# Kernel tuning notes

Hardware: AMD Instinct MI355X
Metric: run time of the kernel (lower is better)

## Reference

```python
import jax, jax.numpy as jnp
import numpy as np


def _ln(x, g, b, eps=1e-5):
    m = jnp.mean(x, axis=-1, keepdims=True)
    v = jnp.mean((x - m) ** 2, axis=-1, keepdims=True)
    return (x - m) / jnp.sqrt(v + eps) * g + b


def _win_part(x, ws):
    # (B,H,W,C) -> (B*nW, ws*ws, C)
    B, H, W, C = x.shape
    x = x.reshape(B, H // ws, ws, W // ws, ws, C)
    x = jnp.transpose(x, (0, 1, 3, 2, 4, 5))
    return x.reshape(-1, ws * ws, C)


def _win_rev(w, ws, H, W):
    # (B*nW, ws, ws, C) -> (B,H,W,C)
    C = w.shape[-1]
    B = w.shape[0] // ((H // ws) * (W // ws))
    x = w.reshape(B, H // ws, W // ws, ws, ws, C)
    x = jnp.transpose(x, (0, 1, 3, 2, 4, 5))
    return x.reshape(B, H, W, C)


def _build_mask(H, W, ws, ss):
    # standard Swin SW-MSA mask, built with numpy at trace time (static shapes)
    img = np.zeros((H, W), np.float32)
    cnt = 0
    for hs in (slice(0, -ws), slice(-ws, -ss), slice(-ss, None)):
        for wsl in (slice(0, -ws), slice(-ws, -ss), slice(-ss, None)):
            img[hs, wsl] = cnt
            cnt += 1
    mw = img.reshape(H // ws, ws, W // ws, ws).transpose(0, 2, 1, 3).reshape(-1, ws * ws)
    diff = mw[:, None, :] - mw[:, :, None]  # (nW, N, N)
    return jnp.asarray(np.where(diff != 0, -np.inf, 0.0).astype(np.float32))


def _swin_block(x, H, W, ws, shift, heads, p):
    B, L, C = x.shape
    hd = C // heads
    N = ws * ws
    shortcut = x
    xg = _ln(x, p['ln1_g'], p['ln1_b']).reshape(B, H, W, C)
    mask = None
    if shift > 0:
        xg = jnp.roll(xg, shift=(-shift, -shift), axis=(1, 2))
        mask = _build_mask(H, W, ws, shift)
    xw = _win_part(xg, ws)  # (B_, N, C)
    qkv = xw @ p['qkv_w'] + p['qkv_b']  # (B_, N, 3C)
    qkv = jnp.transpose(qkv.reshape(-1, N, 3, heads, hd), (2, 0, 3, 1, 4))
    q, k, v = qkv[0] * (hd ** -0.5), qkv[1], qkv[2]  # (B_, h, N, hd)
    attn = jnp.einsum('bhnd,bhmd->bhnm', q, k)
    if mask is not None:
        nW = mask.shape[0]
        attn = attn.reshape(B, nW, heads, N, N) + mask[None, :, None]
        attn = attn.reshape(-1, heads, N, N)
    attn = jax.nn.softmax(attn, axis=-1)
    out = jnp.einsum('bhnm,bhmd->bhnd', attn, v)
    out = jnp.transpose(out, (0, 2, 1, 3)).reshape(-1, N, C)
    out = out @ p['proj_w'] + p['proj_b']
    xg = _win_rev(out.reshape(-1, ws, ws, C), ws, H, W)
    if shift > 0:
        xg = jnp.roll(xg, shift=(shift, shift), axis=(1, 2))
    x = shortcut + xg.reshape(B, L, C)
    h = jax.nn.gelu(_ln(x, p['ln2_g'], p['ln2_b']) @ p['fc1_w'] + p['fc1_b'], approximate=False)
    return x + (h @ p['fc2_w'] + p['fc2_b'])


def _patch_merge(x, H, W, g, b, w):
    B, L, C = x.shape
    xg = x.reshape(B, H, W, C)
    xc = jnp.concatenate([xg[:, 0::2, 0::2], xg[:, 1::2, 0::2], xg[:, 0::2, 1::2], xg[:, 1::2, 1::2]], axis=-1)
    xc = xc.reshape(B, (H // 2) * (W // 2), 4 * C)
    return _ln(xc, g, b) @ w


def setup_inputs() -> dict:
    key = jax.random.key(0)
    ks = jax.random.split(key, 16)
    B, H, W, C = 8, 96, 96, 128
    s = 0.02
    d = {'x': jax.random.normal(ks[0], (B, H * W, C), jnp.float32)}
    i = 1
    for pre in ('a_', 'b_'):
        d[pre + 'ln1_g'] = jnp.ones((C,), jnp.float32)
        d[pre + 'ln1_b'] = jnp.zeros((C,), jnp.float32)
        d[pre + 'qkv_w'] = s * jax.random.normal(ks[i], (C, 3 * C), jnp.float32); i += 1
        d[pre + 'qkv_b'] = jnp.zeros((3 * C,), jnp.float32)
        d[pre + 'proj_w'] = s * jax.random.normal(ks[i], (C, C), jnp.float32); i += 1
        d[pre + 'proj_b'] = jnp.zeros((C,), jnp.float32)
        d[pre + 'ln2_g'] = jnp.ones((C,), jnp.float32)
        d[pre + 'ln2_b'] = jnp.zeros((C,), jnp.float32)
        d[pre + 'fc1_w'] = s * jax.random.normal(ks[i], (C, 4 * C), jnp.float32); i += 1
        d[pre + 'fc1_b'] = jnp.zeros((4 * C,), jnp.float32)
        d[pre + 'fc2_w'] = s * jax.random.normal(ks[i], (4 * C, C), jnp.float32); i += 1
        d[pre + 'fc2_b'] = jnp.zeros((C,), jnp.float32)
    d['mln_g'] = jnp.ones((4 * C,), jnp.float32)
    d['mln_b'] = jnp.zeros((4 * C,), jnp.float32)
    d['red_w'] = s * jax.random.normal(ks[i], (4 * C, 2 * C), jnp.float32)
    d['H'] = H
    d['W'] = W
    return d


def reference(x, a_ln1_g, a_ln1_b, a_qkv_w, a_qkv_b, a_proj_w, a_proj_b, a_ln2_g, a_ln2_b, a_fc1_w, a_fc1_b, a_fc2_w, a_fc2_b, b_ln1_g, b_ln1_b, b_qkv_w, b_qkv_b, b_proj_w, b_proj_b, b_ln2_g, b_ln2_b, b_fc1_w, b_fc1_b, b_fc2_w, b_fc2_b, mln_g, mln_b, red_w, H, W):
    heads, ws = 4, 8
    pa = dict(ln1_g=a_ln1_g, ln1_b=a_ln1_b, qkv_w=a_qkv_w, qkv_b=a_qkv_b, proj_w=a_proj_w, proj_b=a_proj_b, ln2_g=a_ln2_g, ln2_b=a_ln2_b, fc1_w=a_fc1_w, fc1_b=a_fc1_b, fc2_w=a_fc2_w, fc2_b=a_fc2_b)
    pb = dict(ln1_g=b_ln1_g, ln1_b=b_ln1_b, qkv_w=b_qkv_w, qkv_b=b_qkv_b, proj_w=b_proj_w, proj_b=b_proj_b, ln2_g=b_ln2_g, ln2_b=b_ln2_b, fc1_w=b_fc1_w, fc1_b=b_fc1_b, fc2_w=b_fc2_w, fc2_b=b_fc2_b)
    x = _swin_block(x, H, W, ws, 0, heads, pa)          # W-MSA
    x = _swin_block(x, H, W, ws, ws // 2, heads, pb)     # SW-MSA
    return _patch_merge(x, H, W, mln_g, mln_b, red_w)    # (B, HW/4, 2C)
```

## Files before the change

### kernel.cpp

```cpp
#include <hip/hip_runtime.h>
#include <hip/hip_bf16.h>

typedef __bf16 bf16_t;
typedef __bf16 bf16x2 __attribute__((ext_vector_type(2)));
typedef __bf16 bf16x8 __attribute__((ext_vector_type(8)));
typedef float floatx4 __attribute__((ext_vector_type(4)));

#define NTOK 73728
#define LNS 136

__device__ __forceinline__ void gl16(const bf16_t* g, bf16_t* l) {
    __builtin_amdgcn_global_load_lds((const __attribute__((address_space(1))) void*)g,
                                     (__attribute__((address_space(3))) void*)l, 16, 0, 0);
}

__device__ __forceinline__ void stage_ln(const float* __restrict__ src, const float* __restrict__ g,
                                         const float* __restrict__ bta, bf16_t* lnA, int tid) {
    int r = tid >> 2, q = tid & 3;
    const float* rowp = src + (size_t)r * 128 + q * 32;
    float4 v[8];
    float s = 0.0f, sq = 0.0f;
    #pragma unroll
    for (int i = 0; i < 8; i++) {
        v[i] = *(const float4*)(rowp + i * 4);
        s += v[i].x + v[i].y + v[i].z + v[i].w;
        sq += v[i].x * v[i].x + v[i].y * v[i].y + v[i].z * v[i].z + v[i].w * v[i].w;
    }
    s += __shfl_xor(s, 1, 64); sq += __shfl_xor(sq, 1, 64);
    s += __shfl_xor(s, 2, 64); sq += __shfl_xor(sq, 2, 64);
    float m = s * (1.0f / 128.0f);
    float inv = rsqrtf(sq * (1.0f / 128.0f) - m * m + 1e-5f);
    bf16_t* dst = lnA + r * LNS + q * 32;
    #pragma unroll
    for (int i = 0; i < 4; i++) {
        float4 a = v[2 * i], b = v[2 * i + 1];
        float4 g0 = *(const float4*)(g + q * 32 + i * 8);
        float4 g1 = *(const float4*)(g + q * 32 + i * 8 + 4);
        float4 b0 = *(const float4*)(bta + q * 32 + i * 8);
        float4 b1 = *(const float4*)(bta + q * 32 + i * 8 + 4);
        bf16x8 o;
        o[0] = (bf16_t)((a.x - m) * inv * g0.x + b0.x);
        o[1] = (bf16_t)((a.y - m) * inv * g0.y + b0.y);
        o[2] = (bf16_t)((a.z - m) * inv * g0.z + b0.z);
        o[3] = (bf16_t)((a.w - m) * inv * g0.w + b0.w);
        o[4] = (bf16_t)((b.x - m) * inv * g1.x + b1.x);
        o[5] = (bf16_t)((b.y - m) * inv * g1.y + b1.y);
        o[6] = (bf16_t)((b.z - m) * inv * g1.z + b1.z);
        o[7] = (bf16_t)((b.w - m) * inv * g1.w + b1.w);
        *(bf16x8*)(dst + i * 8) = o;
    }
}

struct TPack {
    const float* src[9];
    bf16_t* dst[9];
    int K[9], N[9];
};
__global__ __launch_bounds__(256) void kconv_frag(TPack p) {
    int seg = blockIdx.y;
    int K = p.K[seg], N = p.N[seg];
    int idx = blockIdx.x * 256 + threadIdx.x;
    if (idx >= K * N) return;
    int j = idx & 7;
    int lane = (idx >> 3) & 63;
    int blk = idx >> 9;
    int tilesK = K >> 5;
    int ntile = blk / tilesK, kc = blk - ntile * tilesK;
    int n = ntile * 16 + (lane & 15);
    int k = kc * 32 + (lane >> 4) * 8 + j;
    p.dst[seg][idx] = (bf16_t)p.src[seg][(size_t)k * N + n];
}

__global__ __launch_bounds__(256, 4) void kqkv(const float* __restrict__ X,
                                               const float* __restrict__ g, const float* __restrict__ bta,
                                               const bf16_t* __restrict__ Wf,
                                               const float* __restrict__ bias,
                                               bf16_t* __restrict__ out) {
    alignas(16) __shared__ bf16_t lA[64 * LNS];
    const int tid = threadIdx.x;
    const int rowA = blockIdx.y * 64;
    const int rowB = blockIdx.x * 128;
    stage_ln(X + (size_t)rowA * 128, g, bta, lA, tid);
    __syncthreads();
    const int lane = tid & 63, wv = tid >> 6;
    const int wm = (wv & 1) * 32, wn = (wv >> 1) * 64;
    const int frow = lane & 15, fq = lane >> 4;
    const bf16_t* pw = Wf + (size_t)((rowB + wn) >> 4) * 4 * 512 + lane * 8;
    floatx4 acc[2][4] = {};
    #pragma unroll
    for (int kc = 0; kc < 4; kc++) {
        bf16x8 af[2], bfr[4];
        #pragma unroll
        for (int j = 0; j < 4; j++)
            bfr[j] = *(const bf16x8*)(pw + (j * 4 + kc) * 512);
        #pragma unroll
        for (int i = 0; i < 2; i++)
            af[i] = *(const bf16x8*)&lA[(wm + i * 16 + frow) * LNS + kc * 32 + fq * 8];
        #pragma unroll
        for (int i = 0; i < 2; i++)
            #pragma unroll
            for (int j = 0; j < 4; j++)
                acc[i][j] = __builtin_amdgcn_mfma_f32_16x16x32_bf16(af[i], bfr[j], acc[i][j], 0, 0, 0);
    }
    #pragma unroll
    for (int i = 0; i < 2; i++)
        #pragma unroll
        for (int j = 0; j < 4; j++) {
            int col = rowB + wn + j * 16 + frow;
            float bs = bias[col];
            #pragma unroll
            for (int r = 0; r < 4; r++) {
                int row = rowA + wm + i * 16 + fq * 4 + r;
                out[(size_t)row * 384 + col] = (bf16_t)(acc[i][j][r] + bs);
            }
        }
}

__global__ __launch_bounds__(256, 4) void kmlp(float* __restrict__ res,
                                               const float* __restrict__ g, const float* __restrict__ bta,
                                               const bf16_t* __restrict__ W1f,
                                               const float* __restrict__ b1,
                                               const bf16_t* __restrict__ W2f,
                                               const float* __restrict__ b2) {
    alignas(16) __shared__ bf16_t lA[64 * LNS];
    alignas(16) __shared__ bf16_t lH[64 * LNS];
    const int tid = threadIdx.x;
    const int rowA = blockIdx.x * 64;
    const int lane = tid & 63, wv = tid >> 6;
    const int wm = (wv & 1) * 32, wn = (wv >> 1) * 64;
    const int frow = lane & 15, fq = lane >> 4;
    stage_ln(res + (size_t)rowA * 128, g, bta, lA, tid);
    const bf16_t* pw1 = W1f + (size_t)(wn >> 4) * 4 * 512 + lane * 8;
    const bf16_t* pw2 = W2f + (size_t)(wn >> 4) * 16 * 512 + lane * 8;
    floatx4 accO[2][4] = {};
    for (int cn = 0; cn < 4; cn++) {
        __syncthreads();
        floatx4 accH[2][4] = {};
        #pragma unroll
        for (int kc = 0; kc < 4; kc++) {
            bf16x8 af[2], bfr[4];
            #pragma unroll
            for (int j = 0; j < 4; j++)
                bfr[j] = *(const bf16x8*)(pw1 + (size_t)(cn * 8 * 4 + j * 4 + kc) * 512);
            #pragma unroll
            for (int i = 0; i < 2; i++)
                af[i] = *(const bf16x8*)&lA[(wm + i * 16 + frow) * LNS + kc * 32 + fq * 8];
            #pragma unroll
            for (int i = 0; i < 2; i++)
                #pragma unroll
                for (int j = 0; j < 4; j++)
                    accH[i][j] = __builtin_amdgcn_mfma_f32_16x16x32_bf16(af[i], bfr[j], accH[i][j], 0, 0, 0);
        }
        #pragma unroll
        for (int j = 0; j < 4; j++) {
            int col = wn + j * 16 + frow;
            float bs = b1[cn * 128 + col];
            #pragma unroll
            for (int i = 0; i < 2; i++)
                #pragma unroll
                for (int r = 0; r < 4; r++) {
                    int row = wm + i * 16 + fq * 4 + r;
                    float v = accH[i][j][r] + bs;
                    float u = 1.5957691216057308f * (v + 0.044715f * v * v * v);
                    lH[row * LNS + col] = (bf16_t)(v / (1.0f + __expf(-u)));
                }
        }
        __syncthreads();
        #pragma unroll
        for (int kc = 0; kc < 4; kc++) {
            bf16x8 af[2], bfr[4];
            #pragma unroll
            for (int j = 0; j < 4; j++)
                bfr[j] = *(const bf16x8*)(pw2 + (size_t)(j * 16 + cn * 4 + kc) * 512);
            #pragma unroll
            for (int i = 0; i < 2; i++)
                af[i] = *(const bf16x8*)&lH[(wm + i * 16 + frow) * LNS + kc * 32 + fq * 8];
            #pragma unroll
            for (int i = 0; i < 2; i++)
                #pragma unroll
                for (int j = 0; j < 4; j++)
                    accO[i][j] = __builtin_amdgcn_mfma_f32_16x16x32_bf16(af[i], bfr[j], accO[i][j], 0, 0, 0);
        }
    }
    #pragma unroll
    for (int j = 0; j < 4; j++) {
        int col = wn + j * 16 + frow;
        float bs = b2[col];
        #pragma unroll
        for (int i = 0; i < 2; i++)
            #pragma unroll
            for (int r = 0; r < 4; r++) {
                int row = rowA + wm + i * 16 + fq * 4 + r;
                size_t off = (size_t)row * 128 + col;
                res[off] = res[off] + accO[i][j][r] + bs;
            }
    }
}

template<int MODE>
__global__ __launch_bounds__(256, 4) void gemm64x128(const bf16_t* __restrict__ A,
                                                     const bf16_t* __restrict__ Bf,
                                                     const float* __restrict__ bias,
                                                     const float* __restrict__ res,
                                                     float* __restrict__ outf,
                                                     int M, int N, int K) {
    alignas(16) __shared__ bf16_t lA[2 * 64 * 32];
    const int tid = threadIdx.x;
    const int lane = tid & 63;
    const int wv = tid >> 6;
    const int wm = (wv & 1) * 32;
    const int wn = (wv >> 1) * 64;
    const int frow = lane & 15, fq = lane >> 4;
    const int rowA = blockIdx.y * 64;
    const int rowB = blockIdx.x * 128;
    const int sr = tid >> 2, sc = (tid & 3) * 8;
    const int tilesK = K >> 5;
    const bf16_t* pa = A + (size_t)(rowA + sr) * K + sc;
    const bf16_t* pb = Bf + (size_t)((rowB + wn) >> 4) * tilesK * 512 + lane * 8;
    floatx4 acc[2][4] = {};
    for (int k0 = 0; k0 < K; k0 += 64) {
        __syncthreads();
        gl16(pa + k0,      &lA[tid * 8]);
        gl16(pa + k0 + 32, &lA[2048 + tid * 8]);
        __syncthreads();
        #pragma unroll
        for (int s = 0; s < 2; s++) {
            int kcg = (k0 >> 5) + s;
            bf16x8 af[2], bfr[4];
            #pragma unroll
            for (int j = 0; j < 4; j++)
                bfr[j] = *(const bf16x8*)(pb + (size_t)(j * tilesK + kcg) * 512);
            #pragma unroll
            for (int i = 0; i < 2; i++)
                af[i] = *(const bf16x8*)&lA[s * 2048 + (wm + i * 16 + frow) * 32 + fq * 8];
            #pragma unroll
            for (int i = 0; i < 2; i++)
                #pragma unroll
                for (int j = 0; j < 4; j++)
                    acc[i][j] = __builtin_amdgcn_mfma_f32_16x16x32_bf16(af[i], bfr[j], acc[i][j], 0, 0, 0);
        }
    }
    #pragma unroll
    for (int i = 0; i < 2; i++) {
        #pragma unroll
        for (int j = 0; j < 4; j++) {
            int col = rowB + wn + j * 16 + frow;
            float bs = (MODE == 3) ? 0.0f : bias[col];
            #pragma unroll
            for (int r = 0; r < 4; r++) {
                int row = rowA + wm + i * 16 + fq * 4 + r;
                float v = acc[i][j][r] + bs;
                size_t off = (size_t)row * N + col;
                if (MODE == 1) {
                    outf[off] = res[off] + v;
                } else {
                    outf[off] = v;
                }
            }
        }
    }
}

__global__ __launch_bounds__(256) void kmergeln(const float* __restrict__ x, const float* __restrict__ g,
                                                const float* __restrict__ bta, bf16_t* __restrict__ out) {
    int row = blockIdx.x * 4 + (threadIdx.x >> 6);
    int lane = threadIdx.x & 63;
    int b = row / 2304; int rr = row - b * 2304;
    int i2 = rr / 48, j2 = rr - i2 * 48;
    int q = lane >> 4;
    int cc = (lane & 15) * 8;
    int di = q & 1, dj = q >> 1;
    int src = ((b * 96 + i2 * 2 + di) * 96 + (j2 * 2 + dj)) * 128 + cc;
    float4 a0 = *(const float4*)&x[src];
    float4 a1 = *(const float4*)&x[src + 4];
    float s  = a0.x + a0.y + a0.z + a0.w + a1.x + a1.y + a1.z + a1.w;
    float sq = a0.x*a0.x + a0.y*a0.y + a0.z*a0.z + a0.w*a0.w
             + a1.x*a1.x + a1.y*a1.y + a1.z*a1.z + a1.w*a1.w;
    #pragma unroll
    for (int d = 1; d < 64; d <<= 1) { s += __shfl_xor(s, d, 64); sq += __shfl_xor(sq, d, 64); }
    float m = s * (1.0f / 512.0f);
    float var = sq * (1.0f / 512.0f) - m * m;
    float inv = 1.0f / sqrtf(var + 1e-5f);
    int c = q * 128 + cc;
    float4 g0 = *(const float4*)&g[c];
    float4 g1 = *(const float4*)&g[c + 4];
    float4 b0 = *(const float4*)&bta[c];
    float4 b1 = *(const float4*)&bta[c + 4];
    bf16x8 o;
    o[0] = (bf16_t)((a0.x - m) * inv * g0.x + b0.x);
    o[1] = (bf16_t)((a0.y - m) * inv * g0.y + b0.y);
    o[2] = (bf16_t)((a0.z - m) * inv * g0.z + b0.z);
    o[3] = (bf16_t)((a0.w - m) * inv * g0.w + b0.w);
    o[4] = (bf16_t)((a1.x - m) * inv * g1.x + b1.x);
    o[5] = (bf16_t)((a1.y - m) * inv * g1.y + b1.y);
    o[6] = (bf16_t)((a1.z - m) * inv * g1.z + b1.z);
    o[7] = (bf16_t)((a1.w - m) * inv * g1.w + b1.w);
    *(bf16x8*)&out[row * 512 + c] = o;
}

__global__ __launch_bounds__(64) void kattn(const bf16_t* __restrict__ qkv, bf16_t* __restrict__ out, int shift) {
    alignas(16) __shared__ bf16_t lp[64 * 64];
    alignas(16) __shared__ bf16_t lv[64 * 32];
    int blk = blockIdx.x;
    int win = blk >> 2, h = blk & 3;
    int b = win / 144; int wr = win - b * 144;
    int wi = wr / 12, wj = wr - wi * 12;
    int ri0 = wi * 8, rj0 = wj * 8;
    int lane = threadIdx.x;
    auto trow = [&](int n) {
        int oi = ri0 + (n >> 3) + shift; oi = (oi >= 96) ? oi - 96 : oi;
        int oj = rj0 + (n & 7) + shift;  oj = (oj >= 96) ? oj - 96 : oj;
        return (b * 96 + oi) * 96 + oj;
    };
    {
        size_t base = (size_t)trow(lane) * 384 + 256 + h * 32;
        *(uint4*)&lv[lane * 32]      = *(const uint4*)&qkv[base];
        *(uint4*)&lv[lane * 32 + 8]  = *(const uint4*)&qkv[base + 8];
        *(uint4*)&lv[lane * 32 + 16] = *(const uint4*)&qkv[base + 16];
        *(uint4*)&lv[lane * 32 + 24] = *(const uint4*)&qkv[base + 24];
    }
    int frow = lane & 15, fk = (lane >> 4) * 8;
    bf16x8 qf[4], kf[4];
    #pragma unroll
    for (int t = 0; t < 4; t++) {
        size_t rq = (size_t)trow(t * 16 + frow) * 384;
        qf[t] = *(const bf16x8*)&qkv[rq + h * 32 + fk];
        kf[t] = *(const bf16x8*)&qkv[rq + 128 + h * 32 + fk];
    }
    floatx4 S[4][4] = {};
    #pragma unroll
    for (int mt = 0; mt < 4; mt++)
        #pragma unroll
        for (int nt = 0; nt < 4; nt++)
            S[mt][nt] = __builtin_amdgcn_mfma_f32_16x16x32_bf16(qf[mt], kf[nt], S[mt][nt], 0, 0, 0);
    const float scale = 0.17677669529663687f;
    #pragma unroll
    for (int mt = 0; mt < 4; mt++)
        #pragma unroll
        for (int nt = 0; nt < 4; nt++)
            #pragma unroll
            for (int r = 0; r < 4; r++) S[mt][nt][r] *= scale;
    if (shift > 0) {
        auto grpn = [&](int n) {
            int ri = ri0 + (n >> 3), rj = rj0 + (n & 7);
            int gr = (ri < 88) ? 0 : ((ri < 92) ? 1 : 2);
            int gc = (rj < 88) ? 0 : ((rj < 92) ? 1 : 2);
            return gr * 3 + gc;
        };
        int gk[4];
        #pragma unroll
        for (int nt = 0; nt < 4; nt++) gk[nt] = grpn(nt * 16 + frow);
        #pragma unroll
        for (int mt = 0; mt < 4; mt++)
            #pragma unroll
            for (int r = 0; r < 4; r++) {
                int gq = grpn(mt * 16 + (lane >> 4) * 4 + r);
                #pragma unroll
                for (int nt = 0; nt < 4; nt++)
                    if (gq != gk[nt]) S[mt][nt][r] = -1e30f;
            }
    }
    #pragma unroll
    for (int mt = 0; mt < 4; mt++) {
        #pragma unroll
        for (int r = 0; r < 4; r++) {
            float mx = fmaxf(fmaxf(S[mt][0][r], S[mt][1][r]), fmaxf(S[mt][2][r], S[mt][3][r]));
            #pragma unroll
            for (int d = 1; d < 16; d <<= 1) mx = fmaxf(mx, __shfl_xor(mx, d, 64));
            float sm = 0.0f;
            #pragma unroll
            for (int nt = 0; nt < 4; nt++) {
                float p = __expf(S[mt][nt][r] - mx);
                S[mt][nt][r] = p;
                sm += p;
            }
            #pragma unroll
            for (int d = 1; d < 16; d <<= 1) sm += __shfl_xor(sm, d, 64);
            float inv = 1.0f / sm;
            #pragma unroll
            for (int nt = 0; nt < 4; nt++) S[mt][nt][r] *= inv;
        }
    }
    #pragma unroll
    for (int mt = 0; mt < 4; mt++)
        #pragma unroll
        for (int nt = 0; nt < 4; nt++)
            #pragma unroll
            for (int r = 0; r < 4; r++)
                lp[(mt * 16 + (lane >> 4) * 4 + r) * 64 + nt * 16 + frow] = (bf16_t)S[mt][nt][r];
    __syncthreads();
    floatx4 O[4][2] = {};
    #pragma unroll
    for (int ks = 0; ks < 2; ks++) {
        bf16x8 vbs[2];
        #pragma unroll
        for (int nt = 0; nt < 2; nt++)
            #pragma unroll
            for (int j = 0; j < 8; j++)
                vbs[nt][j] = lv[(ks * 32 + fk + j) * 32 + nt * 16 + frow];
        #pragma unroll
        for (int mt = 0; mt < 4; mt++) {
            bf16x8 pa = *(const bf16x8*)&lp[(mt * 16 + frow) * 64 + ks * 32 + fk];
            #pragma unroll
            for (int nt = 0; nt < 2; nt++)
                O[mt][nt] = __builtin_amdgcn_mfma_f32_16x16x32_bf16(pa, vbs[nt], O[mt][nt], 0, 0, 0);
        }
    }
    #pragma unroll
    for (int mt = 0; mt < 4; mt++) {
        #pragma unroll
        for (int r = 0; r < 4; r++) {
            int qr = mt * 16 + (lane >> 4) * 4 + r;
            size_t orow = (size_t)trow(qr) * 128 + h * 32;
            #pragma unroll
            for (int nt = 0; nt < 2; nt++)
                out[orow + nt * 16 + frow] = (bf16_t)O[mt][nt][r];
        }
    }
}

extern "C" void kernel_launch(void* const* d_in, const int* in_sizes, int n_in,
                              void* d_out, int out_size, void* d_ws, size_t ws_size,
                              hipStream_t stream) {
    const float* x       = (const float*)d_in[0];
    const float* a_ln1g  = (const float*)d_in[1];
    const float* a_ln1b  = (const float*)d_in[2];
    const float* a_qkvw  = (const float*)d_in[3];
    const float* a_qkvb  = (const float*)d_in[4];
    const float* a_projw = (const float*)d_in[5];
    const float* a_projb = (const float*)d_in[6];
    const float* a_ln2g  = (const float*)d_in[7];
    const float* a_ln2b  = (const float*)d_in[8];
    const float* a_fc1w  = (const float*)d_in[9];
    const float* a_fc1b  = (const float*)d_in[10];
    const float* a_fc2w  = (const float*)d_in[11];
    const float* a_fc2b  = (const float*)d_in[12];
    const float* b_ln1g  = (const float*)d_in[13];
    const float* b_ln1b  = (const float*)d_in[14];
    const float* b_qkvw  = (const float*)d_in[15];
    const float* b_qkvb  = (const float*)d_in[16];
    const float* b_projw = (const float*)d_in[17];
    const float* b_projb = (const float*)d_in[18];
    const float* b_ln2g  = (const float*)d_in[19];
    const float* b_ln2b  = (const float*)d_in[20];
    const float* b_qkvw2 = nullptr; (void)b_qkvw2;
    const float* b_fc1w  = (const float*)d_in[21];
    const float* b_fc1b  = (const float*)d_in[22];
    const float* b_fc2w  = (const float*)d_in[23];
    const float* b_fc2b  = (const float*)d_in[24];
    const float* mlng    = (const float*)d_in[25];
    const float* mlnb    = (const float*)d_in[26];
    const float* redw    = (const float*)d_in[27];
    float* out = (float*)d_out;

    char* p = (char*)d_ws;
    float*  buf_x   = (float*)p;  p += (size_t)NTOK * 128 * 4;
    bf16_t* buf_qkv = (bf16_t*)p; p += (size_t)NTOK * 384 * 2;
    bf16_t* buf_attn= (bf16_t*)p; p += (size_t)NTOK * 128 * 2;
    bf16_t* buf_mrg = (bf16_t*)p; p += (size_t)18432 * 512 * 2;
    bf16_t* wt      = (bf16_t*)p;
    bf16_t* aqkvF  = wt;
    bf16_t* aprojF = aqkvF  + 384 * 128;
    bf16_t* afc1F  = aprojF + 128 * 128;
    bf16_t* afc2F  = afc1F  + 512 * 128;
    bf16_t* bqkvF  = afc2F  + 128 * 512;
    bf16_t* bprojF = bqkvF  + 384 * 128;
    bf16_t* bfc1F  = bprojF + 128 * 128;
    bf16_t* bfc2F  = bfc1F  + 512 * 128;
    bf16_t* redF   = bfc2F  + 128 * 512;

    TPack tp;
    const float* srcs[9] = {a_qkvw, a_projw, a_fc1w, a_fc2w, b_qkvw, b_projw, b_fc1w, b_fc2w, redw};
    bf16_t* dsts[9] = {aqkvF, aprojF, afc1F, afc2F, bqkvF, bprojF, bfc1F, bfc2F, redF};
    int Ks[9] = {128, 128, 128, 512, 128, 128, 128, 512, 512};
    int Ns[9] = {384, 128, 512, 128, 384, 128, 512, 128, 256};
    for (int i = 0; i < 9; i++) { tp.src[i] = srcs[i]; tp.dst[i] = dsts[i]; tp.K[i] = Ks[i]; tp.N[i] = Ns[i]; }
    kconv_frag<<<dim3(512, 9), dim3(256), 0, stream>>>(tp);

    const dim3 blk256(256);
    const int MG = NTOK / 64;

    kqkv<<<dim3(3, MG), blk256, 0, stream>>>(x, a_ln1g, a_ln1b, aqkvF, a_qkvb, buf_qkv);
    kattn<<<dim3(1152 * 4), dim3(64), 0, stream>>>(buf_qkv, buf_attn, 0);
    gemm64x128<1><<<dim3(1, MG), blk256, 0, stream>>>(buf_attn, aprojF, a_projb, x, buf_x, NTOK, 128, 128);
    kmlp<<<dim3(MG), blk256, 0, stream>>>(buf_x, a_ln2g, a_ln2b, afc1F, a_fc1b, afc2F, a_fc2b);

    kqkv<<<dim3(3, MG), blk256, 0, stream>>>(buf_x, b_ln1g, b_ln1b, bqkvF, b_qkvb, buf_qkv);
    kattn<<<dim3(1152 * 4), dim3(64), 0, stream>>>(buf_qkv, buf_attn, 4);
    gemm64x128<1><<<dim3(1, MG), blk256, 0, stream>>>(buf_attn, bprojF, b_projb, buf_x, buf_x, NTOK, 128, 128);
    kmlp<<<dim3(MG), blk256, 0, stream>>>(buf_x, b_ln2g, b_ln2b, bfc1F, b_fc1b, bfc2F, b_fc2b);

    kmergeln<<<dim3(18432 / 4), blk256, 0, stream>>>(buf_x, mlng, mlnb, buf_mrg);
    gemm64x128<3><<<dim3(2, 288), blk256, 0, stream>>>(buf_mrg, redF, nullptr, nullptr, out, 18432, 256, 512);
}
```

Before: 463.1 us.

## Remap waves to row strips so GEMM kernels drop block barriers

Changes the per-wave tiling in kqkv and kmlp from a 2x2 split (32 rows x 64 cols) to four row strips (16 rows x all 128 cols). Each wave then reads only the LDS rows it staged itself, which lets the __syncthreads calls be removed. The projection GEMM is replaced by a specialized kproj kernel with the same layout. It loads A via global_load_lds and an explicit vmcnt wait instead of a barrier. In exchange, each wave fetches twice as many weight fragments from global/L2 and holds more B-fragment registers.

```diff
diff --git a/kernel.cpp b/kernel.cpp
--- a/kernel.cpp
+++ b/kernel.cpp
@@ -13,6 +13,7 @@
     __builtin_amdgcn_global_load_lds((const __attribute__((address_space(1))) void*)g,
                                      (__attribute__((address_space(3))) void*)l, 16, 0, 0);
 }
+__device__ __forceinline__ void wait_vm0() { asm volatile("s_waitcnt vmcnt(0)" ::: "memory"); }
 
 __device__ __forceinline__ void stage_ln(const float* __restrict__ src, const float* __restrict__ g,
                                          const float* __restrict__ bta, bf16_t* lnA, int tid) {
@@ -81,39 +82,32 @@
     const int rowA = blockIdx.y * 64;
     const int rowB = blockIdx.x * 128;
     stage_ln(X + (size_t)rowA * 128, g, bta, lA, tid);
-    __syncthreads();
     const int lane = tid & 63, wv = tid >> 6;
-    const int wm = (wv & 1) * 32, wn = (wv >> 1) * 64;
+    const int wm = wv * 16;
     const int frow = lane & 15, fq = lane >> 4;
-    const bf16_t* pw = Wf + (size_t)((rowB + wn) >> 4) * 4 * 512 + lane * 8;
-    floatx4 acc[2][4] = {};
+    const bf16_t* pw = Wf + (size_t)(rowB >> 4) * 4 * 512 + lane * 8;
+    floatx4 acc[8] = {};
     #pragma unroll
     for (int kc = 0; kc < 4; kc++) {
-        bf16x8 af[2], bfr[4];
-        #pragma unroll
-        for (int j = 0; j < 4; j++)
-            bfr[j] = *(const bf16x8*)(pw + (j * 4 + kc) * 512);
-        #pragma unroll
-        for (int i = 0; i < 2; i++)
-            af[i] = *(const bf16x8*)&lA[(wm + i * 16 + frow) * LNS + kc * 32 + fq * 8];
-        #pragma unroll
-        for (int i = 0; i < 2; i++)
-            #pragma unroll
-            for (int j = 0; j < 4; j++)
-                acc[i][j] = __builtin_amdgcn_mfma_f32_16x16x32_bf16(af[i], bfr[j], acc[i][j], 0, 0, 0);
-    }
-    #pragma unroll
-    for (int i = 0; i < 2; i++)
-        #pragma unroll
-        for (int j = 0; j < 4; j++) {
-            int col = rowB + wn + j * 16 + frow;
-            float bs = bias[col];
-            #pragma unroll
-            for (int r = 0; r < 4; r++) {
-                int row = rowA + wm + i * 16 + fq * 4 + r;
-                out[(size_t)row * 384 + col] = (bf16_t)(acc[i][j][r] + bs);
-            }
-        }
+        bf16x8 af = *(const bf16x8*)&lA[(wm + frow) * LNS + kc * 32 + fq * 8];
+        bf16x8 bfr[8];
+        #pragma unroll
+        for (int j = 0; j < 8; j++)
+            bfr[j] = *(const bf16x8*)(pw + (size_t)(j * 4 + kc) * 512);
+        #pragma unroll
+        for (int j = 0; j < 8; j++)
+            acc[j] = __builtin_amdgcn_mfma_f32_16x16x32_bf16(af, bfr[j], acc[j], 0, 0, 0);
+    }
+    #pragma unroll
+    for (int j = 0; j < 8; j++) {
+        int col = rowB + j * 16 + frow;
+        float bs = bias[col];
+        #pragma unroll
+        for (int r = 0; r < 4; r++) {
+            int row = rowA + wm + fq * 4 + r;
+            out[(size_t)row * 384 + col] = (bf16_t)(acc[j][r] + bs);
+        }
+    }
 }
 
 __global__ __launch_bounds__(256, 4) void kmlp(float* __restrict__ res,
@@ -127,83 +121,110 @@
     const int tid = threadIdx.x;
     const int rowA = blockIdx.x * 64;
     const int lane = tid & 63, wv = tid >> 6;
-    const int wm = (wv & 1) * 32, wn = (wv >> 1) * 64;
+    const int wm = wv * 16;
     const int frow = lane & 15, fq = lane >> 4;
     stage_ln(res + (size_t)rowA * 128, g, bta, lA, tid);
-    const bf16_t* pw1 = W1f + (size_t)(wn >> 4) * 4 * 512 + lane * 8;
-    const bf16_t* pw2 = W2f + (size_t)(wn >> 4) * 16 * 512 + lane * 8;
-    floatx4 accO[2][4] = {};
+    const bf16_t* pw1 = W1f + lane * 8;
+    const bf16_t* pw2 = W2f + lane * 8;
+    floatx4 accO[8] = {};
     for (int cn = 0; cn < 4; cn++) {
-        __syncthreads();
-        floatx4 accH[2][4] = {};
+        floatx4 accH[8] = {};
         #pragma unroll
         for (int kc = 0; kc < 4; kc++) {
-            bf16x8 af[2], bfr[4];
-            #pragma unroll
-            for (int j = 0; j < 4; j++)
-                bfr[j] = *(const bf16x8*)(pw1 + (size_t)(cn * 8 * 4 + j * 4 + kc) * 512);
-            #pragma unroll
-            for (int i = 0; i < 2; i++)
-                af[i] = *(const bf16x8*)&lA[(wm + i * 16 + frow) * LNS + kc * 32 + fq * 8];
-            #pragma unroll
-            for (int i = 0; i < 2; i++)
-                #pragma unroll
-                for (int j = 0; j < 4; j++)
-                    accH[i][j] = __builtin_amdgcn_mfma_f32_16x16x32_bf16(af[i], bfr[j], accH[i][j], 0, 0, 0);
-        }
-        #pragma unroll
-        for (int j = 0; j < 4; j++) {
-            int col = wn + j * 16 + frow;
+            bf16x8 af = *(const bf16x8*)&lA[(wm + frow) * LNS + kc * 32 + fq * 8];
+            bf16x8 bfr[8];
+            #pragma unroll
+            for (int j = 0; j < 8; j++)
+                bfr[j] = *(const bf16x8*)(pw1 + (size_t)((cn * 8 + j) * 4 + kc) * 512);
+            #pragma unroll
+            for (int j = 0; j < 8; j++)
+                accH[j] = __builtin_amdgcn_mfma_f32_16x16x32_bf16(af, bfr[j], accH[j], 0, 0, 0);
+        }
+        #pragma unroll
+        for (int j = 0; j < 8; j++) {
+            int col = j * 16 + frow;
             float bs = b1[cn * 128 + col];
             #pragma unroll
-            for (int i = 0; i < 2; i++)
-                #pragma unroll
-                for (int r = 0; r < 4; r++) {
-                    int row = wm + i * 16 + fq * 4 + r;
-                    float v = accH[i][j][r] + bs;
-                    float u = 1.5957691216057308f * (v + 0.044715f * v * v * v);
-                    lH[row * LNS + col] = (bf16_t)(v / (1.0f + __expf(-u)));
-                }
-        }
-        __syncthreads();
+            for (int r = 0; r < 4; r++) {
+                int row = wm + fq * 4 + r;
+                float v = accH[j][r] + bs;
+                float u = 1.5957691216057308f * (v + 0.044715f * v * v * v);
+                lH[row * LNS + col] = (bf16_t)(v / (1.0f + __expf(-u)));
+            }
+        }
         #pragma unroll
         for (int kc = 0; kc < 4; kc++) {
-            bf16x8 af[2], bfr[4];
-            #pragma unroll
-            for (int j = 0; j < 4; j++)
+            bf16x8 af = *(const bf16x8*)&lH[(wm + frow) * LNS + kc * 32 + fq * 8];
+            bf16x8 bfr[8];
+            #pragma unroll
+            for (int j = 0; j < 8; j++)
                 bfr[j] = *(const bf16x8*)(pw2 + (size_t)(j * 16 + cn * 4 + kc) * 512);
             #pragma unroll
-            for (int i = 0; i < 2; i++)
-                af[i] = *(const bf16x8*)&lH[(wm + i * 16 + frow) * LNS + kc * 32 + fq * 8];
-            #pragma unroll
-            for (int i = 0; i < 2; i++)
-                #pragma unroll
-                for (int j = 0; j < 4; j++)
-                    accO[i][j] = __builtin_amdgcn_mfma_f32_16x16x32_bf16(af[i], bfr[j], accO[i][j], 0, 0, 0);
-        }
-    }
-    #pragma unroll
-    for (int j = 0; j < 4; j++) {
-        int col = wn + j * 16 + frow;
+            for (int j = 0; j < 8; j++)
+                accO[j] = __builtin_amdgcn_mfma_f32_16x16x32_bf16(af, bfr[j], accO[j], 0, 0, 0);
+        }
+    }
+    #pragma unroll
+    for (int j = 0; j < 8; j++) {
+        int col = j * 16 + frow;
         float bs = b2[col];
         #pragma unroll
-        for (int i = 0; i < 2; i++)
-            #pragma unroll
-            for (int r = 0; r < 4; r++) {
-                int row = rowA + wm + i * 16 + fq * 4 + r;
-                size_t off = (size_t)row * 128 + col;
-                res[off] = res[off] + accO[i][j][r] + bs;
-            }
-    }
-}
-
-template<int MODE>
-__global__ __launch_bounds__(256, 4) void gemm64x128(const bf16_t* __restrict__ A,
-                                                     const bf16_t* __restrict__ Bf,
-                                                     const float* __restrict__ bias,
-                                                     const float* __restrict__ res,
-                                                     float* __restrict__ outf,
-                                                     int M, int N, int K) {
+        for (int r = 0; r < 4; r++) {
+            int row = rowA + wm + fq * 4 + r;
+            size_t off = (size_t)row * 128 + col;
+            res[off] = res[off] + accO[j][r] + bs;
+        }
+    }
+}
+
+__global__ __launch_bounds__(256, 4) void kproj(const bf16_t* __restrict__ A,
+                                                const bf16_t* __restrict__ Wf,
+                                                const float* __restrict__ bias,
+                                                const float* __restrict__ res,
+                                                float* __restrict__ outf) {
+    alignas(16) __shared__ bf16_t lA[4 * 64 * 32];
+    const int tid = threadIdx.x;
+    const int rowA = blockIdx.x * 64;
+    const int sr = tid >> 2, sc = (tid & 3) * 8;
+    const bf16_t* pa = A + (size_t)(rowA + sr) * 128 + sc;
+    gl16(pa,      &lA[tid * 8]);
+    gl16(pa + 32, &lA[2048 + tid * 8]);
+    gl16(pa + 64, &lA[4096 + tid * 8]);
+    gl16(pa + 96, &lA[6144 + tid * 8]);
+    const int lane = tid & 63, wv = tid >> 6;
+    const int wm = wv * 16;
+    const int frow = lane & 15, fq = lane >> 4;
+    const bf16_t* pw = Wf + lane * 8;
+    wait_vm0();
+    floatx4 acc[8] = {};
+    #pragma unroll
+    for (int kc = 0; kc < 4; kc++) {
+        bf16x8 af = *(const bf16x8*)&lA[kc * 2048 + (wm + frow) * 32 + fq * 8];
+        bf16x8 bfr[8];
+        #pragma unroll
+        for (int j = 0; j < 8; j++)
+            bfr[j] = *(const bf16x8*)(pw + (size_t)(j * 4 + kc) * 512);
+        #pragma unroll
+        for (int j = 0; j < 8; j++)
+            acc[j] = __builtin_amdgcn_mfma_f32_16x16x32_bf16(af, bfr[j], acc[j], 0, 0, 0);
+    }
+    #pragma unroll
+    for (int j = 0; j < 8; j++) {
+        int col = j * 16 + frow;
+        float bs = bias[col];
+        #pragma unroll
+        for (int r = 0; r < 4; r++) {
+            int row = rowA + wm + fq * 4 + r;
+            size_t off = (size_t)row * 128 + col;
+            outf[off] = res[off] + acc[j][r] + bs;
+        }
+    }
+}
+
+__global__ __launch_bounds__(256, 4) void gemmred(const bf16_t* __restrict__ A,
+                                                  const bf16_t* __restrict__ Bf,
+                                                  float* __restrict__ outf,
+                                                  int M, int N, int K) {
     alignas(16) __shared__ bf16_t lA[2 * 64 * 32];
     const int tid = threadIdx.x;
     const int lane = tid & 63;
@@ -241,24 +262,16 @@
         }
     }
     #pragma unroll
-    for (int i = 0; i < 2; i++) {
+    for (int i = 0; i < 2; i++)
         #pragma unroll
         for (int j = 0; j < 4; j++) {
             int col = rowB + wn + j * 16 + frow;
-            float bs = (MODE == 3) ? 0.0f : bias[col];
             #pragma unroll
             for (int r = 0; r < 4; r++) {
                 int row = rowA + wm + i * 16 + fq * 4 + r;
-                float v = acc[i][j][r] + bs;
-                size_t off = (size_t)row * N + col;
-                if (MODE == 1) {
-                    outf[off] = res[off] + v;
-                } else {
-                    outf[off] = v;
-                }
+                outf[(size_t)row * N + col] = acc[i][j][r];
             }
         }
-    }
 }
 
 __global__ __launch_bounds__(256) void kmergeln(const float* __restrict__ x, const float* __restrict__ g,
@@ -443,7 +456,6 @@
     const float* b_projb = (const float*)d_in[18];
     const float* b_ln2g  = (const float*)d_in[19];
     const float* b_ln2b  = (const float*)d_in[20];
-    const float* b_qkvw2 = nullptr; (void)b_qkvw2;
     const float* b_fc1w  = (const float*)d_in[21];
     const float* b_fc1b  = (const float*)d_in[22];
     const float* b_fc2w  = (const float*)d_in[23];
@@ -482,14 +494,14 @@
 
     kqkv<<<dim3(3, MG), blk256, 0, stream>>>(x, a_ln1g, a_ln1b, aqkvF, a_qkvb, buf_qkv);
     kattn<<<dim3(1152 * 4), dim3(64), 0, stream>>>(buf_qkv, buf_attn, 0);
-    gemm64x128<1><<<dim3(1, MG), blk256, 0, stream>>>(buf_attn, aprojF, a_projb, x, buf_x, NTOK, 128, 128);
+    kproj<<<dim3(MG), blk256, 0, stream>>>(buf_attn, aprojF, a_projb, x, buf_x);
     kmlp<<<dim3(MG), blk256, 0, stream>>>(buf_x, a_ln2g, a_ln2b, afc1F, a_fc1b, afc2F, a_fc2b);
 
     kqkv<<<dim3(3, MG), blk256, 0, stream>>>(buf_x, b_ln1g, b_ln1b, bqkvF, b_qkvb, buf_qkv);
     kattn<<<dim3(1152 * 4), dim3(64), 0, stream>>>(buf_qkv, buf_attn, 4);
-    gemm64x128<1><<<dim3(1, MG), blk256, 0, stream>>>(buf_attn, bprojF, b_projb, buf_x, buf_x, NTOK, 128, 128);
+    kproj<<<dim3(MG), blk256, 0, stream>>>(buf_attn, bprojF, b_projb, buf_x, buf_x);
     kmlp<<<dim3(MG), blk256, 0, stream>>>(buf_x, b_ln2g, b_ln2b, bfc1F, b_fc1b, bfc2F, b_fc2b);
 
     kmergeln<<<dim3(18432 / 4), blk256, 0, stream>>>(buf_x, mlng, mlnb, buf_mrg);
-    gemm64x128<3><<<dim3(2, 288), blk256, 0, stream>>>(buf_mrg, redF, nullptr, nullptr, out, 18432, 256, 512);
-}
+    gemmred<<<dim3(2, 288), blk256, 0, stream>>>(buf_mrg, redF, out, 18432, 256, 512);
+}
```

New measurement: 517.7 us. 11.8% more time.
